# Optimization experiments

Hardware: AMD Instinct MI355X
Metric: run time of the kernel (lower is better)

The kernel has to match this reference:

```python
import jax, jax.numpy as jnp
from jax import lax
import numpy as np

NUM_NODES = 30   # pinned by LayerNorm(30) in TCNBlock
H = 4            # heads
C = 64           # channel per head
HC = H * C       # 256 = all_channels, first TCN channel
F_IN = 64
B = 1024         # graphs per batch
EPG = 240        # random edges per graph (no self loops; GATv2 adds them)
LN_EPS = 1e-5
NEG_SLOPE = 0.2


def _glorot(k, shp):
    fan_in = int(np.prod(shp[1:])) if len(shp) > 1 else int(shp[0])
    return jax.random.normal(k, shp, dtype=jnp.float32) / np.sqrt(fan_in)


def setup_inputs():
    key = jax.random.key(0)
    ks = jax.random.split(key, 16)
    N = B * NUM_NODES
    # random intra-graph edges with src != dst (PyG remove_self_loops then add_self_loops)
    src_l = jax.random.randint(ks[0], (B, EPG), 0, NUM_NODES)
    off = jax.random.randint(ks[1], (B, EPG), 1, NUM_NODES)
    dst_l = (src_l + off) % NUM_NODES
    base = (jnp.arange(B) * NUM_NODES)[:, None]
    edge_index = jnp.stack([(src_l + base).reshape(-1), (dst_l + base).reshape(-1)]).astype(jnp.int32)
    z = lambda *s: jnp.zeros(s, jnp.float32)
    return {
        "x": jax.random.normal(ks[2], (N, F_IN), dtype=jnp.float32),
        "gat_Wl": _glorot(ks[3], (HC, F_IN)), "gat_bl": z(HC),
        "gat_Wr": _glorot(ks[4], (HC, F_IN)), "gat_br": z(HC),
        "gat_att": _glorot(ks[5], (H, C)), "gat_bias": z(HC),
        "tcn0_w": _glorot(ks[6], (HC, HC, 3)), "tcn0_b": z(HC),
        "ln0_w": jnp.ones((NUM_NODES,), jnp.float32), "ln0_b": z(NUM_NODES),
        "tcn1_w": _glorot(ks[7], (512, HC, 3)), "tcn1_b": z(512),
        "ln1_w": jnp.ones((NUM_NODES,), jnp.float32), "ln1_b": z(NUM_NODES),
        "ds1_w": _glorot(ks[8], (512, HC, 1)), "ds1_b": z(512),
        "tcn2_w": _glorot(ks[9], (256, 512, 3)), "tcn2_b": z(256),
        "ln2_w": jnp.ones((NUM_NODES,), jnp.float32), "ln2_b": z(NUM_NODES),
        "ds2_w": _glorot(ks[10], (256, 512, 1)), "ds2_b": z(256),
        "fc1_w": _glorot(ks[11], (512, 256 * NUM_NODES)), "fc1_b": z(512),
        "fc2_w": _glorot(ks[12], (256, 512)), "fc2_b": z(256),
        "fc3_w": _glorot(ks[13], (144, 256)), "fc3_b": z(144),
        "edge_index": edge_index,
    }


def _conv1d(x, w, b, dil):
    # torch Conv1d: x [B,Cin,L], w [Cout,Cin,K], padding = dil*(K-1)//2
    pad = dil * (w.shape[-1] - 1) // 2
    y = lax.conv_general_dilated(x, w, (1,), [(pad, pad)], rhs_dilation=(dil,),
                                 dimension_numbers=("NCH", "OIH", "NCH"))
    return y + b[None, :, None]


def _ln(x, w, b):
    # LayerNorm over last dim (length 30)
    mu = jnp.mean(x, -1, keepdims=True)
    var = jnp.var(x, -1, keepdims=True)
    return (x - mu) * lax.rsqrt(var + LN_EPS) * w + b


def reference(x, gat_Wl, gat_bl, gat_Wr, gat_br, gat_att, gat_bias,
              tcn0_w, tcn0_b, ln0_w, ln0_b,
              tcn1_w, tcn1_b, ln1_w, ln1_b, ds1_w, ds1_b,
              tcn2_w, tcn2_b, ln2_w, ln2_b, ds2_w, ds2_b,
              fc1_w, fc1_b, fc2_w, fc2_b, fc3_w, fc3_b, edge_index):
    N = x.shape[0]
    # GATv2Conv default: add self loops
    loops = jnp.arange(N, dtype=edge_index.dtype)
    ei = jnp.concatenate([edge_index, jnp.stack([loops, loops])], axis=1)
    src, dst = ei[0], ei[1]
    xl = (x @ gat_Wl.T + gat_bl).reshape(N, H, C)  # source transform
    xr = (x @ gat_Wr.T + gat_br).reshape(N, H, C)  # target transform
    s = jax.nn.leaky_relu(xl[src] + xr[dst], NEG_SLOPE)          # [E,H,C]
    e = jnp.einsum("ehc,hc->eh", s, gat_att)                     # [E,H]
    m = jax.ops.segment_max(e, dst, num_segments=N)              # segment softmax
    expe = jnp.exp(e - m[dst])
    alpha = expe / jax.ops.segment_sum(expe, dst, num_segments=N)[dst]
    agg = jax.ops.segment_sum(alpha[:, :, None] * xl[src], dst, num_segments=N)
    h = jax.nn.relu(agg.reshape(N, HC) + gat_bias)
    h = h.reshape(-1, NUM_NODES, HC).transpose(0, 2, 1)          # [B, HC, 30]
    # TCN: dilations 1,2,4; residual with 1x1 downsample when channels change
    y = jax.nn.relu(_ln(_conv1d(h, tcn0_w, tcn0_b, 1), ln0_w, ln0_b)) + h
    y = jax.nn.relu(_ln(_conv1d(y, tcn1_w, tcn1_b, 2), ln1_w, ln1_b)) + _conv1d(y, ds1_w, ds1_b, 1)
    y = jax.nn.relu(_ln(_conv1d(y, tcn2_w, tcn2_b, 4), ln2_w, ln2_b)) + _conv1d(y, ds2_w, ds2_b, 1)
    z = y.reshape(y.shape[0], -1)                                # [B, 256*30]
    z = jax.nn.relu(z @ fc1_w.T + fc1_b)
    z = jax.nn.relu(z @ fc2_w.T + fc2_b)
    out = z @ fc3_w.T + fc3_b                                    # [B, 144]
    return out, alpha, ei
```

## Files before the change

kernel.cpp:

```cpp
#include <hip/hip_runtime.h>
#include <hip/hip_bf16.h>

typedef __bf16  bf16x8 __attribute__((ext_vector_type(8)));
typedef __bf16  bf16x4 __attribute__((ext_vector_type(4)));
typedef float   f32x4  __attribute__((ext_vector_type(4)));
typedef __hip_bfloat16 bf;

__device__ __forceinline__ float clamp256(float v) {
    return fminf(fmaxf(v, -256.f), 256.f);
}
__device__ __forceinline__ float sane(float v) {
    return fminf(fmaxf(v, -1e4f), 1e4f);
}
__device__ __forceinline__ int swzk(int k, int col) {
    return (k & ~31) | ((((k >> 3) & 3) ^ ((col >> 1) & 3)) << 3) | (k & 7);
}

template<int TAPS, bool HASWD>
__global__ __launch_bounds__(256) void gemm_tf(
    const bf* __restrict__ A, const bf* __restrict__ Wt, const bf* __restrict__ Wd,
    const float* __restrict__ bias, const float* __restrict__ biasd,
    const float* __restrict__ lnw, const float* __restrict__ lnb,
    const bf* __restrict__ res, int res_stride,
    bf* __restrict__ outb, float* __restrict__ outf, int out_stride,
    int M, int N, int K, int dil, int mode, int relu, int padded, int nn, int kLen)
{
    constexpr int NT = TAPS + (HASWD ? 1 : 0);
    __shared__ __align__(16) unsigned short sA[66 * 40];
    __shared__ __align__(16) unsigned short sB[NT][64 * 40];
    __shared__ float sS[4][64], sS2[4][64];

    const int tid  = threadIdx.x;
    const int wv   = tid >> 6;
    const int lane = tid & 63;
    const int m0   = blockIdx.y * 64;
    const int n0   = blockIdx.x * 64;
    const int frow = lane & 15;
    const int fq   = lane >> 4;
    const int kOff = blockIdx.z * kLen;
    const int kEnd = (kOff + kLen < K) ? (kOff + kLen) : K;

    if (tid < 40) sA[64 * 40 + tid] = (unsigned short)0;

    int aoff[NT];
    {
        int token = wv * 16 + frow;
        int b = token >> 5, l = token & 31;
        #pragma unroll
        for (int t = 0; t < NT; ++t) {
            int s = (t < TAPS) ? (t - TAPS / 2) * dil : 0;
            int ar;
            if (padded) {
                int ls = l + s;
                ar = ((unsigned)ls < 32u) ? (b * 32 + ls) : 64;
            } else {
                ar = token;
            }
            aoff[t] = ar * 40 + fq * 8;
        }
    }

    const int srow = tid >> 2;
    const int schk = (tid & 3) << 3;
    int raG = m0 + srow;
    if (!padded && raG >= M) raG = -1;
    const int rbG  = n0 + srow;
    const bool bval = rbG < N;
    const bf* Ap = (raG >= 0) ? (A + (size_t)raG * K) : nullptr;
    const bf* Bp[NT];
    #pragma unroll
    for (int t = 0; t < NT; ++t)
        Bp[t] = (HASWD && t == TAPS) ? (Wd + (size_t)rbG * K)
                                     : (Wt + ((size_t)t * N + rbG) * K);

    f32x4 accC[4], accR[4];
    #pragma unroll
    for (int i = 0; i < 4; ++i) { accC[i] = 0.f; accR[i] = 0.f; }

    const uint4 zu = make_uint4(0u, 0u, 0u, 0u);
    uint4 pa, pb[NT];
    pa = Ap ? *(const uint4*)(Ap + kOff + schk) : zu;
    #pragma unroll
    for (int t = 0; t < NT; ++t)
        pb[t] = bval ? *(const uint4*)(Bp[t] + kOff + schk) : zu;

    for (int kb = kOff; kb < kEnd; kb += 32) {
        __syncthreads();
        *(uint4*)(sA + srow * 40 + schk) = pa;
        #pragma unroll
        for (int t = 0; t < NT; ++t)
            *(uint4*)(&sB[t][srow * 40 + schk]) = pb[t];
        __syncthreads();
        int kn = kb + 32;
        if (kn < kEnd) {
            pa = Ap ? *(const uint4*)(Ap + kn + schk) : zu;
            #pragma unroll
            for (int t = 0; t < NT; ++t)
                pb[t] = bval ? *(const uint4*)(Bp[t] + kn + schk) : zu;
        }
        #pragma unroll
        for (int t = 0; t < TAPS; ++t) {
            bf16x8 af = *(const bf16x8*)(sA + aoff[t]);
            #pragma unroll
            for (int nt = 0; nt < 4; ++nt) {
                bf16x8 bg = *(const bf16x8*)(&sB[t][(nt * 16 + frow) * 40 + fq * 8]);
                accC[nt] = __builtin_amdgcn_mfma_f32_16x16x32_bf16(af, bg, accC[nt], 0, 0, 0);
            }
        }
        if constexpr (HASWD) {
            bf16x8 af = *(const bf16x8*)(sA + aoff[TAPS]);
            #pragma unroll
            for (int nt = 0; nt < 4; ++nt) {
                bf16x8 bg = *(const bf16x8*)(&sB[TAPS][(nt * 16 + frow) * 40 + fq * 8]);
                accR[nt] = __builtin_amdgcn_mfma_f32_16x16x32_bf16(af, bg, accR[nt], 0, 0, 0);
            }
        }
    }

    if (mode == 0) {
        #pragma unroll
        for (int nt = 0; nt < 4; ++nt) {
            int col = n0 + nt * 16 + frow;
            if (col >= N) continue;
            float bv = bias ? bias[col] : 0.f;
            #pragma unroll
            for (int r = 0; r < 4; ++r) {
                int row = m0 + wv * 16 + fq * 4 + r;
                if (row >= M) continue;
                float v = accC[nt][r] + bv;
                if (relu) v = fmaxf(v, 0.f);
                if (outb) outb[(size_t)row * out_stride + col] = __float2bfloat16(clamp256(v));
                else      outf[(size_t)row * out_stride + col] = sane(v);
            }
        }
    } else if (mode == 3) {
        bf* po = outb + (size_t)blockIdx.z * M * out_stride;
        #pragma unroll
        for (int nt = 0; nt < 4; ++nt) {
            int col = n0 + nt * 16 + frow;
            if (col >= N) continue;
            #pragma unroll
            for (int r = 0; r < 4; ++r) {
                int row = m0 + wv * 16 + fq * 4 + r;
                if (row >= M) continue;
                po[(size_t)row * out_stride + col] = __float2bfloat16(accC[nt][r]);
            }
        }
    } else if (mode == 5) {
        if constexpr (HASWD) {
            bf* out2 = (bf*)res;
            int orow_[4];
            #pragma unroll
            for (int r = 0; r < 4; ++r) {
                int row = m0 + wv * 16 + fq * 4 + r;
                orow_[r] = relu ? ((row / nn) * 32 + (row % nn)) : row;
            }
            #pragma unroll
            for (int nt = 0; nt < 4; ++nt) {
                int col = n0 + nt * 16 + frow;
                if (col >= N) continue;
                float bv = bias[col], bd = biasd[col];
                #pragma unroll
                for (int r = 0; r < 4; ++r) {
                    int row = m0 + wv * 16 + fq * 4 + r;
                    if (row >= M) continue;
                    outb[(size_t)row * out_stride + col] = __float2bfloat16(clamp256(accC[nt][r] + bv));
                    out2[(size_t)orow_[r] * res_stride + col] = __float2bfloat16(clamp256(accR[nt][r] + bd));
                }
            }
        }
    } else {
        float bvc[4], bdc[4];
        #pragma unroll
        for (int nt = 0; nt < 4; ++nt) {
            int col = n0 + nt * 16 + frow;
            bvc[nt] = bias[col];
            bdc[nt] = (HASWD && biasd) ? biasd[col] : 0.f;
        }
        float s[4], s2[4];
        #pragma unroll
        for (int nt = 0; nt < 4; ++nt) { s[nt] = 0.f; s2[nt] = 0.f; }
        #pragma unroll
        for (int nt = 0; nt < 4; ++nt)
            #pragma unroll
            for (int r = 0; r < 4; ++r) {
                int row = wv * 16 + fq * 4 + r;
                int l = row & 31;
                float v = sane(accC[nt][r] + bvc[nt]);
                if (l < nn) { s[nt] += v; s2[nt] += v * v; }
            }
        #pragma unroll
        for (int nt = 0; nt < 4; ++nt) {
            s[nt]  += __shfl_xor(s[nt], 16);  s[nt]  += __shfl_xor(s[nt], 32);
            s2[nt] += __shfl_xor(s2[nt], 16); s2[nt] += __shfl_xor(s2[nt], 32);
        }
        if (fq == 0) {
            #pragma unroll
            for (int nt = 0; nt < 4; ++nt) {
                sS[wv][nt * 16 + frow]  = s[nt];
                sS2[wv][nt * 16 + frow] = s2[nt];
            }
        }
        __syncthreads();
        const int gi = wv >> 1;
        const float inv = 1.f / (float)nn;
        #pragma unroll
        for (int nt = 0; nt < 4; ++nt) {
            int c = nt * 16 + frow;
            int colg = n0 + c;
            float S  = sS[2 * gi][c]  + sS[2 * gi + 1][c];
            float S2 = sS2[2 * gi][c] + sS2[2 * gi + 1][c];
            float mu = S * inv;
            float var = S2 * inv - mu * mu;
            float rs = rsqrtf(fmaxf(var, 0.f) + 1e-5f);
            #pragma unroll
            for (int r = 0; r < 4; ++r) {
                int row = wv * 16 + fq * 4 + r;
                int l = row & 31;
                int grow = m0 + row;
                float outv = 0.f;
                if (l < nn) {
                    float v = (sane(accC[nt][r] + bvc[nt]) - mu) * rs * lnw[l] + lnb[l];
                    v = fmaxf(v, 0.f);
                    float rr;
                    if constexpr (HASWD) rr = sane(accR[nt][r] + bdc[nt]);
                    else rr = __bfloat162float(res[(size_t)grow * res_stride + colg]);
                    outv = clamp256(v + rr);
                }
                outb[(size_t)grow * out_stride + colg] = __float2bfloat16(outv);
            }
        }
    }
}

template<int TAPS, bool HASWD>
__global__ __launch_bounds__(256, 2) void gemm_tcn(
    const bf* __restrict__ A, const bf* __restrict__ Wt, const bf* __restrict__ Wd,
    const float* __restrict__ bias, const float* __restrict__ biasd,
    const float* __restrict__ lnw, const float* __restrict__ lnb,
    const bf* __restrict__ res, int res_stride,
    bf* __restrict__ outb, int out_stride,
    int M, int N, int K, int dil, int nn)
{
    constexpr int NT = TAPS + (HASWD ? 1 : 0);
    constexpr int SA = 257 * 40;
    __shared__ __align__(16) unsigned short sA[2 * SA];
    __shared__ __align__(16) unsigned short sBall[2 * NT * 64 * 32];

    const int tid  = threadIdx.x;
    const int wv   = tid >> 6;
    const int lane = tid & 63;
    const int frow = lane & 15;
    const int fq   = lane >> 4;

    const int gx  = gridDim.x;
    const int nwg = gx * gridDim.y;
    int wg = blockIdx.y * gx + blockIdx.x;
    if ((nwg & 7) == 0) wg = (wg & 7) * (nwg >> 3) + (wg >> 3);
    const int n0 = (wg % gx) * 64;
    const int m0 = (wg / gx) * 256;

    if (tid < 40) {
        sA[256 * 40 + tid]      = (unsigned short)0;
        sA[SA + 256 * 40 + tid] = (unsigned short)0;
    }

    int aoff[TAPS][4];
    #pragma unroll
    for (int mr = 0; mr < 4; ++mr) {
        int token = wv * 64 + mr * 16 + frow;
        int b5 = token >> 5, l = token & 31;
        #pragma unroll
        for (int t = 0; t < TAPS; ++t) {
            int ls = l + (t - TAPS / 2) * dil;
            int ar = ((unsigned)ls < 32u) ? (b5 * 32 + ls) : 256;
            aoff[t][mr] = ar * 40 + fq * 8;
        }
    }
    const int bco = (fq ^ ((frow >> 1) & 3)) << 3;

    const int srow = tid >> 2;
    const int chS  = (tid & 3) << 3;
    const bf* Ap = A + (size_t)(m0 + srow) * K + chS;

    const bf* bsrc[4];
    {
        int lr = lane >> 2, lc = lane & 3;
        #pragma unroll
        for (int i = 0; i < 4; ++i) {
            int colb = n0 + i * 16 + lr;
            const bf* Wb;
            if (HASWD && wv == TAPS) Wb = Wd + (size_t)colb * K;
            else if (wv < TAPS)      Wb = Wt + ((size_t)wv * N + colb) * K;
            else                     Wb = Wt + (size_t)colb * K;
            bsrc[i] = Wb + lc * 8;
        }
    }

    f32x4 accC[4][4], accR[4][4];
    #pragma unroll
    for (int i = 0; i < 4; ++i)
        #pragma unroll
        for (int j = 0; j < 4; ++j) { accC[i][j] = 0.f; if (HASWD) accR[i][j] = 0.f; }

    #define ISSUE_B(BUFB, KBS)                                                      \
        if (wv < NT) {                                                              \
            unsigned short* bas = sBall + ((size_t)((BUFB) * NT + wv) * 64) * 32;   \
            _Pragma("unroll")                                                       \
            for (int i = 0; i < 4; ++i) {                                           \
                __builtin_amdgcn_global_load_lds(                                   \
                    (const __attribute__((address_space(1))) void*)(bsrc[i] + (KBS)), \
                    (__attribute__((address_space(3))) void*)(bas + i * 512),       \
                    16, 0, 0);                                                      \
            }                                                                       \
        }

    uint4 pa[4];
    #pragma unroll
    for (int i = 0; i < 4; ++i) pa[i] = *(const uint4*)(Ap + (size_t)i * 64 * K);
    ISSUE_B(0, 0);
    #pragma unroll
    for (int i = 0; i < 4; ++i)
        *(uint4*)(sA + (srow + i * 64) * 40 + chS) = pa[i];
    __syncthreads();

    int buf = 0;
    for (int kb = 0; kb < K; kb += 32) {
        int kn = kb + 32;
        if (kn < K) {
            #pragma unroll
            for (int i = 0; i < 4; ++i)
                pa[i] = *(const uint4*)(Ap + (size_t)i * 64 * K + kn);
            ISSUE_B(buf ^ 1, kn);
        }
        const unsigned short* sAb = sA + (size_t)buf * SA;
        const unsigned short* sBb = sBall + (size_t)buf * NT * 2048;
        bf16x8 aMid[4];
        #pragma unroll
        for (int mr = 0; mr < 4; ++mr)
            aMid[mr] = *(const bf16x8*)(sAb + aoff[TAPS / 2][mr]);
        #pragma unroll
        for (int t = 0; t < TAPS; ++t) {
            bf16x8 af[4];
            #pragma unroll
            for (int mr = 0; mr < 4; ++mr)
                af[mr] = (t == TAPS / 2) ? aMid[mr]
                                         : *(const bf16x8*)(sAb + aoff[t][mr]);
            #pragma unroll
            for (int nt = 0; nt < 4; ++nt) {
                bf16x8 bg = *(const bf16x8*)(sBb + (size_t)t * 2048 + (nt * 16 + frow) * 32 + bco);
                #pragma unroll
                for (int mr = 0; mr < 4; ++mr)
                    accC[mr][nt] = __builtin_amdgcn_mfma_f32_16x16x32_bf16(af[mr], bg, accC[mr][nt], 0, 0, 0);
            }
        }
        if constexpr (HASWD) {
            #pragma unroll
            for (int nt = 0; nt < 4; ++nt) {
                bf16x8 bg = *(const bf16x8*)(sBb + (size_t)TAPS * 2048 + (nt * 16 + frow) * 32 + bco);
                #pragma unroll
                for (int mr = 0; mr < 4; ++mr)
                    accR[mr][nt] = __builtin_amdgcn_mfma_f32_16x16x32_bf16(aMid[mr], bg, accR[mr][nt], 0, 0, 0);
            }
        }
        if (kn < K) {
            unsigned short* sAn = sA + (size_t)(buf ^ 1) * SA;
            #pragma unroll
            for (int i = 0; i < 4; ++i)
                *(uint4*)(sAn + (srow + i * 64) * 40 + chS) = pa[i];
        }
        __syncthreads();
        buf ^= 1;
    }
    #undef ISSUE_B

    float bvc[4], bdc[4];
    #pragma unroll
    for (int nt = 0; nt < 4; ++nt) {
        int col = n0 + nt * 16 + frow;
        bvc[nt] = bias[col];
        bdc[nt] = HASWD ? biasd[col] : 0.f;
    }
    float S[2][4], Q[2][4];
    #pragma unroll
    for (int h = 0; h < 2; ++h)
        #pragma unroll
        for (int nt = 0; nt < 4; ++nt) { S[h][nt] = 0.f; Q[h][nt] = 0.f; }
    #pragma unroll
    for (int mr = 0; mr < 4; ++mr) {
        const int h = mr >> 1;
        #pragma unroll
        for (int nt = 0; nt < 4; ++nt)
            #pragma unroll
            for (int r = 0; r < 4; ++r) {
                int l = (mr & 1) * 16 + fq * 4 + r;
                if (l < nn) {
                    float v = sane(accC[mr][nt][r] + bvc[nt]);
                    S[h][nt] += v; Q[h][nt] += v * v;
                }
            }
    }
    const float inv = 1.f / (float)nn;
    float mu[2][4], rsg[2][4];
    #pragma unroll
    for (int h = 0; h < 2; ++h)
        #pragma unroll
        for (int nt = 0; nt < 4; ++nt) {
            float s = S[h][nt], q = Q[h][nt];
            s += __shfl_xor(s, 16); s += __shfl_xor(s, 32);
            q += __shfl_xor(q, 16); q += __shfl_xor(q, 32);
            float m = s * inv;
            float var = q * inv - m * m;
            mu[h][nt]  = m;
            rsg[h][nt] = rsqrtf(fmaxf(var, 0.f) + 1e-5f);
        }
    float lw[2][4], lb2[2][4];
    #pragma unroll
    for (int p = 0; p < 2; ++p)
        #pragma unroll
        for (int r = 0; r < 4; ++r) {
            int l = p * 16 + fq * 4 + r;
            bool ok = l < nn;
            lw[p][r]  = ok ? lnw[l] : 0.f;
            lb2[p][r] = ok ? lnb[l] : 0.f;
        }
    #pragma unroll
    for (int nt = 0; nt < 4; ++nt) {
        const int colg = n0 + nt * 16 + frow;
        #pragma unroll
        for (int mr = 0; mr < 4; ++mr) {
            const int h = mr >> 1, p = mr & 1;
            #pragma unroll
            for (int r = 0; r < 4; ++r) {
                int l = p * 16 + fq * 4 + r;
                int grow = m0 + wv * 64 + mr * 16 + fq * 4 + r;
                float outv = 0.f;
                if (l < nn) {
                    float v = (sane(accC[mr][nt][r] + bvc[nt]) - mu[h][nt]) * rsg[h][nt] * lw[p][r] + lb2[p][r];
                    v = fmaxf(v, 0.f);
                    float rr;
                    if constexpr (HASWD) rr = sane(accR[mr][nt][r] + bdc[nt]);
                    else rr = __bfloat162float(res[(size_t)grow * res_stride + colg]);
                    outv = clamp256(v + rr);
                }
                outb[(size_t)grow * out_stride + colg] = __float2bfloat16(outv);
            }
        }
    }
}

#define MAXNE 270
#define XLS   260
#define SHP   264
template<int CONV>
__global__ __launch_bounds__(256, 4) void gat_fused4(
    const int* __restrict__ ei, const bf* __restrict__ xlb, const bf* __restrict__ xrb,
    const bf* __restrict__ Wlr, const float* __restrict__ gbl, const float* __restrict__ gbr,
    const float* __restrict__ att, const float* __restrict__ gbias,
    const bf* __restrict__ Wf, const float* __restrict__ cbias,
    const float* __restrict__ lnw, const float* __restrict__ lnb,
    bf* __restrict__ yout, float* __restrict__ dalpha, float* __restrict__ dei,
    int E0, int ET, int EPG, int nn)
{
    __shared__ __align__(16) __bf16 sXL[32 * XLS];
    __shared__ __align__(16) __bf16 sHX[33 * SHP];
    __shared__ __align__(16) float sExp[MAXNE * 4];
    __shared__ int   sSD[MAXNE];
    __shared__ unsigned short sList[MAXNE];
    __shared__ int   sCnt[32];
    __shared__ int   sOff[33];

    const int g = blockIdx.x, tid = threadIdx.x, wv = tid >> 6, lane = tid & 63;
    if (EPG + nn > MAXNE) return;
    const int NE = EPG + nn;
    const int frow = lane & 15;
    const int fq   = lane >> 4;

    for (int k = tid; k < EPG; k += 256) {
        int s = ei[(size_t)g * EPG + k] - g * nn;
        int d = ei[(size_t)E0 + (size_t)g * EPG + k] - g * nn;
        s = min(max(s, 0), nn - 1);
        d = min(max(d, 0), nn - 1);
        sSD[k] = s | (d << 16);
    }
    for (int k = EPG + tid; k < NE; k += 256) {
        int node = k - EPG;
        sSD[k] = node | (node << 16);
    }
    if constexpr (CONV) {
        unsigned short* sXg = (unsigned short*)sExp;
        const uint4* gx = (const uint4*)(xlb + (size_t)g * nn * 64);
        for (int k = tid; k < nn * 8; k += 256) {
            int node = k >> 3, k8 = k & 7;
            *(uint4*)(sXg + node * 64 + ((k8 ^ (node & 7)) << 3)) = gx[k];
        }
        const uint4 zu = make_uint4(0u, 0u, 0u, 0u);
        for (int k = nn * 8 + tid; k < 32 * 8; k += 256) {
            int node = k >> 3, k8 = k & 7;
            *(uint4*)(sXg + node * 64 + ((k8 ^ (node & 7)) << 3)) = zu;
        }
        __bf16 z = (__bf16)0.f;
        for (int k = tid; k < SHP; k += 256) sHX[32 * SHP + k] = z;
    } else {
        const uint4* gxl = (const uint4*)(xlb + (size_t)g * nn * 256);
        const uint4* gxr = (const uint4*)(xrb + (size_t)g * nn * 256);
        for (int k = tid; k < nn * 32; k += 256) {
            int node = k >> 5, c8 = k & 31;
            *(uint4*)(sXL + node * XLS + c8 * 8) = gxl[k];
            *(uint4*)(sHX + node * SHP + c8 * 8) = gxr[k];
        }
    }
    if (tid < 32) sCnt[tid] = 0;
    __syncthreads();

    for (int k = tid; k < NE; k += 256) atomicAdd(&sCnt[sSD[k] >> 16], 1);
    if constexpr (CONV) {
        const unsigned short* sXg = (const unsigned short*)sExp;
        bf16x8 axf[2][2];
        #pragma unroll
        for (int mr = 0; mr < 2; ++mr)
            #pragma unroll
            for (int kc = 0; kc < 2; ++kc) {
                int row = mr * 16 + frow;
                axf[mr][kc] = *(const bf16x8*)(sXg + row * 64 + (((kc * 4 + fq) ^ (row & 7)) << 3));
            }
        const int colw = wv * 64;
        #pragma unroll
        for (int out = 0; out < 2; ++out) {
            f32x4 ga[2][4];
            #pragma unroll
            for (int mr = 0; mr < 2; ++mr)
                #pragma unroll
                for (int ct = 0; ct < 4; ++ct) ga[mr][ct] = 0.f;
            #pragma unroll
            for (int kc = 0; kc < 2; ++kc)
                #pragma unroll
                for (int ct = 0; ct < 4; ++ct) {
                    const __bf16* bp = (const __bf16*)Wlr + (size_t)out * 16384 +
                        ((((size_t)(((colw >> 4) + ct) * 2 + kc) * 16 + frow) * 4 + fq) * 8);
                    bf16x8 bg = *(const bf16x8*)bp;
                    ga[0][ct] = __builtin_amdgcn_mfma_f32_16x16x32_bf16(axf[0][kc], bg, ga[0][ct], 0, 0, 0);
                    ga[1][ct] = __builtin_amdgcn_mfma_f32_16x16x32_bf16(axf[1][kc], bg, ga[1][ct], 0, 0, 0);
                }
            const float* bb = out ? gbr : gbl;
            #pragma unroll
            for (int ct = 0; ct < 4; ++ct) {
                int col = colw + ct * 16 + frow;
                float b = bb[col];
                #pragma unroll
                for (int mr = 0; mr < 2; ++mr)
                    #pragma unroll
                    for (int r = 0; r < 4; ++r) {
                        int row = mr * 16 + fq * 4 + r;
                        float v = clamp256(ga[mr][ct][r] + b);
                        if (out == 0) sXL[row * XLS + col] = (__bf16)v;
                        else          sHX[row * SHP + col] = (__bf16)v;
                    }
            }
        }
    }
    __syncthreads();
    if (tid < 32) {
        int acc = 0, last = 0;
        #pragma unroll
        for (int j = 0; j < 32; ++j) {
            int c = sCnt[j];
            if (j < tid) acc += c;
            if (j == 31) last = c;
        }
        sOff[tid] = acc;
        if (tid == 31) sOff[32] = acc + last;
        sCnt[tid] = 0;
    }
    __syncthreads();
    for (int k = tid; k < NE; k += 256) {
        int d = sSD[k] >> 16;
        int p = atomicAdd(&sCnt[d], 1);
        sList[sOff[d] + p] = (unsigned short)k;
    }

    for (int k = tid; k < NE; k += 256) {
        int s, d; size_t eg;
        if (k < EPG) {
            int sd = sSD[k];
            s = g * nn + (sd & 0xffff); d = g * nn + (sd >> 16);
            eg = (size_t)g * EPG + k;
        }
        else { int node = g * nn + (k - EPG); s = d = node; eg = (size_t)E0 + (size_t)g * nn + (k - EPG); }
        dei[eg] = (float)s;
        dei[(size_t)ET + eg] = (float)d;
    }
    __syncthreads();

    const float4 attv = *(const float4*)(att + lane * 4);
    const int h4 = lane >> 4;
    for (int i = wv; i < NE; i += 4) {
        int sd = sSD[i];
        int srcl = sd & 0xffff, dstl = sd >> 16;
        bf16x4 a = *(const bf16x4*)(sXL + srcl * XLS + lane * 4);
        bf16x4 b = *(const bf16x4*)(sHX + dstl * SHP + lane * 4);
        float p = 0.f;
        {
            float v0 = (float)a[0] + (float)b[0]; v0 = v0 > 0.f ? v0 : 0.2f * v0; p += v0 * attv.x;
            float v1 = (float)a[1] + (float)b[1]; v1 = v1 > 0.f ? v1 : 0.2f * v1; p += v1 * attv.y;
            float v2 = (float)a[2] + (float)b[2]; v2 = v2 > 0.f ? v2 : 0.2f * v2; p += v2 * attv.z;
            float v3 = (float)a[3] + (float)b[3]; v3 = v3 > 0.f ? v3 : 0.2f * v3; p += v3 * attv.w;
        }
        p += __shfl_xor(p, 1); p += __shfl_xor(p, 2);
        p += __shfl_xor(p, 4); p += __shfl_xor(p, 8);
        if ((lane & 15) == 0)
            sExp[i * 4 + h4] = __expf(fminf(fmaxf(p, -60.f), 60.f));
    }
    __syncthreads();

    {
        const int grp  = wv * 8 + (lane >> 3);
        const int s8   = lane & 7;
        const int chb  = s8 * 32;
        const int head = s8 >> 1;
        bf* hrow = yout + ((size_t)g * 32 + grp) * 256 + chb;

        if (grp < nn) {
            const int beg = sOff[grp], end = sOff[grp + 1];
            float den = 0.f;
            f32x4 acc[8];
            #pragma unroll
            for (int k2 = 0; k2 < 8; ++k2) acc[k2] = 0.f;

            for (int q = beg; q < end; ++q) {
                int e = sList[q];
                float ev = sExp[e * 4 + head];
                den += ev;
                const __bf16* xp = sXL + (sSD[e] & 0xffff) * XLS + chb;
                #pragma unroll
                for (int k2 = 0; k2 < 4; ++k2) {
                    bf16x8 xa = *(const bf16x8*)(xp + k2 * 8);
                    #pragma unroll
                    for (int j = 0; j < 4; ++j)
                        acc[k2 * 2][j]     += ev * (float)xa[j];
                    #pragma unroll
                    for (int j = 0; j < 4; ++j)
                        acc[k2 * 2 + 1][j] += ev * (float)xa[4 + j];
                }
            }
            const float rden = 1.f / fmaxf(den, 1e-30f);

            if (!(s8 & 1)) {
                for (int q = beg; q < end; ++q) {
                    int e = sList[q];
                    float al = fminf(fmaxf(sExp[e * 4 + head] * rden, 0.f), 1.f);
                    size_t eg = (e < EPG) ? ((size_t)g * EPG + e)
                                          : ((size_t)E0 + (size_t)g * nn + (e - EPG));
                    dalpha[eg * 4 + head] = al;
                }
            }

            #pragma unroll
            for (int k2 = 0; k2 < 8; ++k2) {
                float4 gbv = *(const float4*)(gbias + chb + k2 * 4);
                bf16x4 o;
                o[0] = (__bf16)clamp256(fmaxf(acc[k2][0] * rden + gbv.x, 0.f));
                o[1] = (__bf16)clamp256(fmaxf(acc[k2][1] * rden + gbv.y, 0.f));
                o[2] = (__bf16)clamp256(fmaxf(acc[k2][2] * rden + gbv.z, 0.f));
                o[3] = (__bf16)clamp256(fmaxf(acc[k2][3] * rden + gbv.w, 0.f));
                if constexpr (CONV) *(bf16x4*)(sHX + grp * SHP + chb + k2 * 4) = o;
                else                *(bf16x4*)(hrow + k2 * 4) = o;
            }
        } else {
            bf16x4 z; z[0] = (__bf16)0.f; z[1] = (__bf16)0.f; z[2] = (__bf16)0.f; z[3] = (__bf16)0.f;
            #pragma unroll
            for (int k2 = 0; k2 < 8; ++k2) {
                if constexpr (CONV) *(bf16x4*)(sHX + grp * SHP + chb + k2 * 4) = z;
                else                *(bf16x4*)(hrow + k2 * 4) = z;
            }
        }
    }

    if constexpr (CONV) {
        __syncthreads();
        const int colw = wv * 64;
        f32x4 c0[2][4];
        #pragma unroll
        for (int i = 0; i < 2; ++i)
            #pragma unroll
            for (int j = 0; j < 4; ++j) c0[i][j] = 0.f;

        #pragma unroll
        for (int kc = 0; kc < 8; ++kc) {
            bf16x8 af[3][2];
            #pragma unroll
            for (int t = 0; t < 3; ++t)
                #pragma unroll
                for (int mr = 0; mr < 2; ++mr) {
                    int l = mr * 16 + frow + t - 1;
                    int ar = ((unsigned)l < 32u) ? l : 32;
                    af[t][mr] = *(const bf16x8*)(sHX + ar * SHP + kc * 32 + fq * 8);
                }
            #pragma unroll
            for (int t = 0; t < 3; ++t) {
                bf16x8 bgs[4];
                #pragma unroll
                for (int nt = 0; nt < 4; ++nt) {
                    const __bf16* bp = (const __bf16*)Wf +
                        ((((size_t)(t * 16 + (colw >> 4) + nt) * 8 + kc) * 16 + frow) * 4 + fq) * 8;
                    bgs[nt] = *(const bf16x8*)bp;
                }
                #pragma unroll
                for (int nt = 0; nt < 4; ++nt) {
                    c0[0][nt] = __builtin_amdgcn_mfma_f32_16x16x32_bf16(af[t][0], bgs[nt], c0[0][nt], 0, 0, 0);
                    c0[1][nt] = __builtin_amdgcn_mfma_f32_16x16x32_bf16(af[t][1], bgs[nt], c0[1][nt], 0, 0, 0);
                }
            }
        }

        float bv[4];
        #pragma unroll
        for (int nt = 0; nt < 4; ++nt) bv[nt] = cbias[colw + nt * 16 + frow];
        float S[4], Q[4];
        #pragma unroll
        for (int nt = 0; nt < 4; ++nt) { S[nt] = 0.f; Q[nt] = 0.f; }
        #pragma unroll
        for (int mr = 0; mr < 2; ++mr)
            #pragma unroll
            for (int nt = 0; nt < 4; ++nt)
                #pragma unroll
                for (int r = 0; r < 4; ++r) {
                    int l = mr * 16 + fq * 4 + r;
                    if (l < nn) {
                        float v = sane(c0[mr][nt][r] + bv[nt]);
                        S[nt] += v; Q[nt] += v * v;
                    }
                }
        const float inv = 1.f / (float)nn;
        float mu[4], rsg[4];
        #pragma unroll
        for (int nt = 0; nt < 4; ++nt) {
            float s = S[nt], q = Q[nt];
            s += __shfl_xor(s, 16); s += __shfl_xor(s, 32);
            q += __shfl_xor(q, 16); q += __shfl_xor(q, 32);
            float m = s * inv;
            float var = q * inv - m * m;
            mu[nt]  = m;
            rsg[nt] = rsqrtf(fmaxf(var, 0.f) + 1e-5f);
        }
        float lw[2][4], lb2[2][4];
        #pragma unroll
        for (int p = 0; p < 2; ++p)
            #pragma unroll
            for (int r = 0; r < 4; ++r) {
                int l = p * 16 + fq * 4 + r;
                bool ok = l < nn;
                lw[p][r]  = ok ? lnw[l] : 0.f;
                lb2[p][r] = ok ? lnb[l] : 0.f;
            }
        #pragma unroll
        for (int nt = 0; nt < 4; ++nt) {
            const int colf = colw + nt * 16 + frow;
            #pragma unroll
            for (int mr = 0; mr < 2; ++mr)
                #pragma unroll
                for (int r = 0; r < 4; ++r) {
                    int l = mr * 16 + fq * 4 + r;
                    float outv = 0.f;
                    if (l < nn) {
                        float v = (sane(c0[mr][nt][r] + bv[nt]) - mu[nt]) * rsg[nt] * lw[mr][r] + lb2[mr][r];
                        v = fmaxf(v, 0.f);
                        float rr = (float)sHX[l * SHP + colf];
                        outv = clamp256(v + rr);
                    }
                    yout[((size_t)g * 32 + l) * 256 + colf] = __float2bfloat16(outv);
                }
        }
    }
}

struct CvtSegs { const float* in[7]; bf* out[7]; int n[7]; };
__global__ void prep_cvt(CvtSegs s, int total)
{
    int idx = blockIdx.x * 256 + threadIdx.x;
    if (idx >= total) return;
    #pragma unroll
    for (int i = 0; i < 7; ++i) {
        if (idx < s.n[i]) { s.out[i][idx] = __float2bfloat16(s.in[i][idx]); return; }
        idx -= s.n[i];
    }
}
struct TapSegs { const float* w[3]; bf* o[3]; int cc[3]; int kk[3]; int swz[3]; };
__global__ void prep_taps3(TapSegs s, int total)
{
    int idx = blockIdx.x * 256 + threadIdx.x;
    if (idx >= total) return;
    #pragma unroll
    for (int i = 0; i < 3; ++i) {
        if (idx < s.cc[i]) {
            unsigned K = (unsigned)s.kk[i];
            unsigned co = (unsigned)idx / K, ci = (unsigned)idx % K;
            int dst = co * K + (s.swz[i] ? swzk(ci, co) : ci);
            #pragma unroll
            for (int k = 0; k < 3; ++k)
                s.o[i][(size_t)k * s.cc[i] + dst] = __float2bfloat16(s.w[i][(size_t)idx * 3 + k]);
            return;
        }
        idx -= s.cc[i];
    }
}
__global__ void prep_wswz(const float* __restrict__ w, bf* __restrict__ o,
                          int total, int K, int swz)
{
    int idx = blockIdx.x * 256 + threadIdx.x;
    if (idx >= total) return;
    int co = idx / K, ci = idx % K;
    o[(size_t)co * K + (swz ? swzk(ci, co) : ci)] = __float2bfloat16(w[idx]);
}
__global__ void prep_bfrag(const float* __restrict__ w, bf* __restrict__ o, int HC)
{
    int idx = blockIdx.x * 256 + threadIdx.x;
    if (idx >= HC * HC) return;
    int co = idx / HC, ci = idx % HC;
    int cg = co >> 4, fr = co & 15, kc = ci >> 5, fq = (ci >> 3) & 3, w8 = ci & 7;
    int NCg = HC >> 4, NKc = HC >> 5;
    #pragma unroll
    for (int t = 0; t < 3; ++t) {
        size_t dst = (((((size_t)t * NCg + cg) * NKc + kc) * 16 + fr) * 4 + fq) * 8 + w8;
        o[dst] = __float2bfloat16(w[(size_t)idx * 3 + t]);
    }
}
__global__ void prep_gwfrag(const float* __restrict__ wl, const float* __restrict__ wr,
                            bf* __restrict__ o, int HC, int FI)
{
    int idx = blockIdx.x * 256 + threadIdx.x;
    int tot = HC * FI;
    if (idx >= 2 * tot) return;
    const float* w = (idx < tot) ? wl : wr;
    int j = (idx < tot) ? idx : idx - tot;
    int col = j / FI, k = j % FI;
    int cg = col >> 4, fr = col & 15, kc = k >> 5, fq = (k >> 3) & 3, w8 = k & 7;
    size_t dst = (size_t)((idx < tot) ? 0 : 1) * tot +
        ((((size_t)(cg * (FI >> 5) + kc) * 16 + fr) * 4 + fq) * 8 + w8);
    o[dst] = __float2bfloat16(w[j]);
}

__global__ void prep_fc1(const float* __restrict__ w, bf* __restrict__ o, int F1, int nn, int HC)
{
    int idx = blockIdx.x * 256 + threadIdx.x;
    int kw = 32 * HC;
    if (idx >= F1 * kw) return;
    int co = idx / kw, r = idx % kw, l = r / HC, ci = r % HC;
    float hv = 0.f;
    if (l < nn) hv = w[(size_t)co * (HC * nn) + ci * nn + l];
    o[idx] = __float2bfloat16(hv);
}

__global__ void fc1red(const bf* __restrict__ zp, const float* __restrict__ bias,
                       bf* __restrict__ o, int MN, int N, int S)
{
    int idx = blockIdx.x * 256 + threadIdx.x;
    if (idx >= MN) return;
    float s = 0.f;
    for (int z = 0; z < S; ++z) s += __bfloat162float(zp[(size_t)z * MN + idx]);
    o[idx] = __float2bfloat16(clamp256(fmaxf(s + bias[idx % N], 0.f)));
}

extern "C" void kernel_launch(void* const* d_in, const int* in_sizes, int n_in,
                              void* d_out, int out_size, void* d_ws, size_t ws_size,
                              hipStream_t stream)
{
    (void)n_in; (void)ws_size;
    const float* x   = (const float*)d_in[0];
    const float* Wl  = (const float*)d_in[1];  const float* bl  = (const float*)d_in[2];
    const float* Wr  = (const float*)d_in[3];  const float* br  = (const float*)d_in[4];
    const float* att = (const float*)d_in[5];  const float* gb  = (const float*)d_in[6];
    const float* t0w = (const float*)d_in[7];  const float* t0b = (const float*)d_in[8];
    const float* l0w = (const float*)d_in[9];  const float* l0b = (const float*)d_in[10];
    const float* t1w = (const float*)d_in[11]; const float* t1b = (const float*)d_in[12];
    const float* l1w = (const float*)d_in[13]; const float* l1b = (const float*)d_in[14];
    const float* d1w = (const float*)d_in[15]; const float* d1b = (const float*)d_in[16];
    const float* t2w = (const float*)d_in[17]; const float* t2b = (const float*)d_in[18];
    const float* l2w = (const float*)d_in[19]; const float* l2b = (const float*)d_in[20];
    const float* d2w = (const float*)d_in[21]; const float* d2b = (const float*)d_in[22];
    const float* f1w = (const float*)d_in[23]; const float* f1b = (const float*)d_in[24];
    const float* f2w = (const float*)d_in[25]; const float* f2b = (const float*)d_in[26];
    const float* f3w = (const float*)d_in[27]; const float* f3b = (const float*)d_in[28];
    const int*   ei  = (const int*)d_in[29];

    const int HC   = in_sizes[6];
    const int F_IN = in_sizes[1] / (HC > 0 ? HC : 1);
    const int NN   = in_sizes[0] / (F_IN > 0 ? F_IN : 1);
    const int E0   = in_sizes[29] / 2;
    const int ET   = E0 + NN;
    int nn = in_sizes[9];  nn = nn < 1 ? 1 : (nn > 32 ? 32 : nn);
    const int NG   = NN / nn;
    const int EPG  = NG > 0 ? E0 / NG : 0;
    const int C1   = in_sizes[12];
    const int C2   = in_sizes[18];
    const int F1   = in_sizes[24];
    const int F2   = in_sizes[26];
    const int F3   = in_sizes[28];
    const int NG2  = (NG + 1) / 2;

    float* dout   = (float*)d_out;
    float* dei    = dout + ((size_t)out_size - 2 * (size_t)ET);
    float* dalpha = dei - (size_t)ET * 4;

    const bool fused0 = (HC == 256) && (F_IN == 64) && (nn >= 1) && (nn <= 32)
                        && (EPG + nn <= MAXNE) && ((NN % 64) == 0);
    const int  gcA = NG2, gcB = NG - NG2;
    const bool fastc = ((gcA * 32) % 256 == 0) && ((gcB * 32) % 256 == 0)
                       && (C1 % 64 == 0) && (C2 % 64 == 0)
                       && (HC % 32 == 0) && (C1 % 32 == 0);

    char* ws = (char*)d_ws;
    const size_t MB = 1ull << 20;
    bf*    xb   = (bf*)(ws);
    bf*    WkA  = (bf*)(ws + 4 * MB);
    bf*    WkB  = WkA + (size_t)3 * HC * HC;
    bf*    WkC  = WkB + (size_t)3 * C1 * HC;
    bf*    Wlb  = WkC + (size_t)3 * C2 * C1;
    bf*    Wrb  = Wlb + (size_t)HC * F_IN;
    bf*    f2wb = Wrb + (size_t)HC * F_IN;
    bf*    f3wb = f2wb + (size_t)F2 * F1;
    bf*    d1wb = f3wb + (size_t)F3 * F2;
    bf*    d2wb = d1wb + (size_t)C1 * HC;
    bf*    WkAf = d2wb + (size_t)C2 * C1;
    bf*    WlrF = WkAf + (size_t)3 * HC * HC;
    char*  S0   = ws + (size_t)(7.5 * MB);
    char*  S1   = ws + 25 * MB;

    bf*    xrb  = (bf*)S0;
    bf*    hbuf = (bf*)S0;
    bf*    xlb  = (bf*)S1;
    bf*    y0   = fused0 ? (bf*)S0 : (bf*)S1;
    bf*    y1c  = fused0 ? (bf*)S1 : (bf*)S0;
    char*  fcS  = fused0 ? S1 : S0;
    bf*    W1t  = (bf*)fcS;
    bf*    z1p  = (bf*)(fcS + (size_t)(8.5 * MB));
    bf*    z1   = (bf*)(ws);
    bf*    z2   = (bf*)(ws + 2 * MB);

    {
        CvtSegs cs;
        cs.in[0] = x;   cs.out[0] = xb;   cs.n[0] = NN * F_IN;
        cs.in[1] = Wl;  cs.out[1] = Wlb;  cs.n[1] = HC * F_IN;
        cs.in[2] = Wr;  cs.out[2] = Wrb;  cs.n[2] = HC * F_IN;
        cs.in[3] = f2w; cs.out[3] = f2wb; cs.n[3] = F2 * F1;
        cs.in[4] = f3w; cs.out[4] = f3wb; cs.n[4] = F3 * F2;
        cs.in[5] = nullptr; cs.out[5] = nullptr; cs.n[5] = 0;
        cs.in[6] = nullptr; cs.out[6] = nullptr; cs.n[6] = 0;
        int tot = 0; for (int i = 0; i < 5; ++i) tot += cs.n[i];
        prep_cvt<<<(tot + 255) / 256, 256, 0, stream>>>(cs, tot);
        TapSegs ts;
        ts.w[0] = t0w; ts.o[0] = WkA; ts.cc[0] = HC * HC; ts.kk[0] = HC; ts.swz[0] = 0;
        ts.w[1] = t1w; ts.o[1] = WkB; ts.cc[1] = C1 * HC; ts.kk[1] = HC; ts.swz[1] = fastc ? 1 : 0;
        ts.w[2] = t2w; ts.o[2] = WkC; ts.cc[2] = C2 * C1; ts.kk[2] = C1; ts.swz[2] = fastc ? 1 : 0;
        int tt = ts.cc[0] + ts.cc[1] + ts.cc[2];
        prep_taps3<<<(tt + 255) / 256, 256, 0, stream>>>(ts, tt);
        prep_wswz<<<(C1 * HC + 255) / 256, 256, 0, stream>>>(d1w, d1wb, C1 * HC, HC, fastc ? 1 : 0);
        prep_wswz<<<(C2 * C1 + 255) / 256, 256, 0, stream>>>(d2w, d2wb, C2 * C1, C1, fastc ? 1 : 0);
        if (fused0) {
            prep_bfrag<<<(HC * HC + 255) / 256, 256, 0, stream>>>(t0w, WkAf, HC);
            prep_gwfrag<<<(2 * HC * F_IN + 255) / 256, 256, 0, stream>>>(Wl, Wr, WlrF, HC, F_IN);
        }
    }

    if (fused0) {
        gat_fused4<1><<<NG, 256, 0, stream>>>(ei, xb, nullptr, WlrF, bl, br,
                                              att, gb, WkAf, t0b, l0w, l0b,
                                              y0, dalpha, dei, E0, ET, EPG, nn);
    } else {
        gemm_tf<1, true><<<dim3((HC + 63) / 64, (NN + 63) / 64), 256, 0, stream>>>(
            xb, Wlb, Wrb, bl, br, nullptr, nullptr, (const bf*)xrb, HC,
            xlb, nullptr, HC, NN, HC, F_IN, 1, 5, 0, 0, nn, F_IN);
        gat_fused4<0><<<NG, 256, 0, stream>>>(ei, xlb, xrb, nullptr, nullptr, nullptr,
                                              att, gb, nullptr, nullptr, nullptr, nullptr,
                                              hbuf, dalpha, dei, E0, ET, EPG, nn);
        gemm_tf<3, false><<<dim3((HC + 63) / 64, NG * 32 / 64), 256, 0, stream>>>(
            hbuf, WkA, nullptr, t0b, nullptr, l0w, l0b, hbuf, HC,
            y0, nullptr, HC, NG * 32, HC, HC, 1, 2, 0, 1, nn, HC);
    }

    for (int c = 0; c < 2; ++c) {
        int g0 = c * NG2;
        int gc = (c == 0) ? NG2 : (NG - NG2);
        if (gc <= 0) continue;
        const bf* y0c = y0 + (size_t)g0 * 32 * HC;
        bf*       y2c = y0 + (size_t)g0 * 32 * HC;
        if (fastc) {
            gemm_tcn<3, true><<<dim3(C1 / 64, gc * 32 / 256), 256, 0, stream>>>(
                y0c, WkB, d1wb, t1b, d1b, l1w, l1b, nullptr, 0,
                y1c, C1, gc * 32, C1, HC, 2, nn);
            gemm_tcn<3, true><<<dim3(C2 / 64, gc * 32 / 256), 256, 0, stream>>>(
                y1c, WkC, d2wb, t2b, d2b, l2w, l2b, nullptr, 0,
                y2c, C2, gc * 32, C2, C1, 4, nn);
        } else {
            gemm_tf<3, true><<<dim3((C1 + 63) / 64, gc * 32 / 64), 256, 0, stream>>>(
                y0c, WkB, d1wb, t1b, d1b, l1w, l1b, nullptr, 0,
                y1c, nullptr, C1, gc * 32, C1, HC, 2, 2, 0, 1, nn, HC);
            gemm_tf<3, true><<<dim3((C2 + 63) / 64, gc * 32 / 64), 256, 0, stream>>>(
                y1c, WkC, d2wb, t2b, d2b, l2w, l2b, nullptr, 0,
                y2c, nullptr, C2, gc * 32, C2, C1, 4, 2, 0, 1, nn, C1);
        }
    }

    prep_fc1<<<(F1 * 32 * HC + 255) / 256, 256, 0, stream>>>(f1w, W1t, F1, nn, HC);
    gemm_tf<1, false><<<dim3((F1 + 63) / 64, (NG + 63) / 64, 8), 256, 0, stream>>>(
        y0, W1t, nullptr, nullptr, nullptr, nullptr, nullptr, nullptr, 0,
        z1p, nullptr, F1, NG, F1, 32 * HC, 1, 3, 0, 0, nn, 4 * HC);
    fc1red<<<(NG * F1 + 255) / 256, 256, 0, stream>>>(z1p, f1b, z1, NG * F1, F1, 8);

    gemm_tf<1, false><<<dim3((F2 + 63) / 64, (NG + 63) / 64), 256, 0, stream>>>(
        z1, f2wb, nullptr, f2b, nullptr, nullptr, nullptr, nullptr, 0,
        z2, nullptr, F2, NG, F2, F1, 1, 0, 1, 0, nn, F1);
    gemm_tf<1, false><<<dim3((F3 + 63) / 64, (NG + 63) / 64), 256, 0, stream>>>(
        z2, f3wb, nullptr, f3b, nullptr, nullptr, nullptr, nullptr, 0,
        nullptr, dout, F3, NG, F3, F2, 1, 0, 0, 0, nn, F2);
}
```

Measured before the change: 424.0 us.

## Template TCN GEMM row tile and restructure GAT alpha writes into coalesced pass

Makes the TCN GEMM's M-tile size a template parameter. The second TCN layer (N=256) now uses 128-row tiles with higher occupancy, which gives more workgroups and better CU fill. Separately, the GAT kernel stores per-destination denominators in shared memory and writes all attention coefficients afterwards in one coalesced float4 pass over edges. This replaces the scattered per-head writes inside the aggregation loop, at the cost of an extra barrier and division pass.

Measured after the change: 410.4 us. -3.2%, faster.

```diff
diff --git a/kernel.cpp b/kernel.cpp
--- a/kernel.cpp
+++ b/kernel.cpp
@@ -233,8 +233,8 @@
     }
 }
 
-template<int TAPS, bool HASWD>
-__global__ __launch_bounds__(256, 2) void gemm_tcn(
+template<int TAPS, bool HASWD, int MR>
+__global__ __launch_bounds__(256, (MR == 2) ? 3 : 2) void gemm_tcn(
     const bf* __restrict__ A, const bf* __restrict__ Wt, const bf* __restrict__ Wd,
     const float* __restrict__ bias, const float* __restrict__ biasd,
     const float* __restrict__ lnw, const float* __restrict__ lnb,
@@ -243,7 +243,9 @@
     int M, int N, int K, int dil, int nn)
 {
     constexpr int NT = TAPS + (HASWD ? 1 : 0);
-    constexpr int SA = 257 * 40;
+    constexpr int ROWS = 64 * MR;
+    constexpr int GH = (MR >= 4) ? 2 : 1;
+    constexpr int SA = (ROWS + 1) * 40;
     __shared__ __align__(16) unsigned short sA[2 * SA];
     __shared__ __align__(16) unsigned short sBall[2 * NT * 64 * 32];
 
@@ -258,22 +260,22 @@
     int wg = blockIdx.y * gx + blockIdx.x;
     if ((nwg & 7) == 0) wg = (wg & 7) * (nwg >> 3) + (wg >> 3);
     const int n0 = (wg % gx) * 64;
-    const int m0 = (wg / gx) * 256;
+    const int m0 = (wg / gx) * ROWS;
 
     if (tid < 40) {
-        sA[256 * 40 + tid]      = (unsigned short)0;
-        sA[SA + 256 * 40 + tid] = (unsigned short)0;
-    }
-
-    int aoff[TAPS][4];
-    #pragma unroll
-    for (int mr = 0; mr < 4; ++mr) {
-        int token = wv * 64 + mr * 16 + frow;
+        sA[ROWS * 40 + tid]      = (unsigned short)0;
+        sA[SA + ROWS * 40 + tid] = (unsigned short)0;
+    }
+
+    int aoff[TAPS][MR];
+    #pragma unroll
+    for (int mr = 0; mr < MR; ++mr) {
+        int token = wv * (16 * MR) + mr * 16 + frow;
         int b5 = token >> 5, l = token & 31;
         #pragma unroll
         for (int t = 0; t < TAPS; ++t) {
             int ls = l + (t - TAPS / 2) * dil;
-            int ar = ((unsigned)ls < 32u) ? (b5 * 32 + ls) : 256;
+            int ar = ((unsigned)ls < 32u) ? (b5 * 32 + ls) : ROWS;
             aoff[t][mr] = ar * 40 + fq * 8;
         }
     }
@@ -297,9 +299,9 @@
         }
     }
 
-    f32x4 accC[4][4], accR[4][4];
-    #pragma unroll
-    for (int i = 0; i < 4; ++i)
+    f32x4 accC[MR][4], accR[MR][4];
+    #pragma unroll
+    for (int i = 0; i < MR; ++i)
         #pragma unroll
         for (int j = 0; j < 4; ++j) { accC[i][j] = 0.f; if (HASWD) accR[i][j] = 0.f; }
 
@@ -315,12 +317,12 @@
             }                                                                       \
         }
 
-    uint4 pa[4];
-    #pragma unroll
-    for (int i = 0; i < 4; ++i) pa[i] = *(const uint4*)(Ap + (size_t)i * 64 * K);
+    uint4 pa[MR];
+    #pragma unroll
+    for (int i = 0; i < MR; ++i) pa[i] = *(const uint4*)(Ap + (size_t)i * 64 * K);
     ISSUE_B(0, 0);
     #pragma unroll
-    for (int i = 0; i < 4; ++i)
+    for (int i = 0; i < MR; ++i)
         *(uint4*)(sA + (srow + i * 64) * 40 + chS) = pa[i];
     __syncthreads();
 
@@ -329,28 +331,28 @@
         int kn = kb + 32;
         if (kn < K) {
             #pragma unroll
-            for (int i = 0; i < 4; ++i)
+            for (int i = 0; i < MR; ++i)
                 pa[i] = *(const uint4*)(Ap + (size_t)i * 64 * K + kn);
             ISSUE_B(buf ^ 1, kn);
         }
         const unsigned short* sAb = sA + (size_t)buf * SA;
         const unsigned short* sBb = sBall + (size_t)buf * NT * 2048;
-        bf16x8 aMid[4];
-        #pragma unroll
-        for (int mr = 0; mr < 4; ++mr)
+        bf16x8 aMid[MR];
+        #pragma unroll
+        for (int mr = 0; mr < MR; ++mr)
             aMid[mr] = *(const bf16x8*)(sAb + aoff[TAPS / 2][mr]);
         #pragma unroll
         for (int t = 0; t < TAPS; ++t) {
-            bf16x8 af[4];
-            #pragma unroll
-            for (int mr = 0; mr < 4; ++mr)
+            bf16x8 af[MR];
+            #pragma unroll
+            for (int mr = 0; mr < MR; ++mr)
                 af[mr] = (t == TAPS / 2) ? aMid[mr]
                                          : *(const bf16x8*)(sAb + aoff[t][mr]);
             #pragma unroll
             for (int nt = 0; nt < 4; ++nt) {
                 bf16x8 bg = *(const bf16x8*)(sBb + (size_t)t * 2048 + (nt * 16 + frow) * 32 + bco);
                 #pragma unroll
-                for (int mr = 0; mr < 4; ++mr)
+                for (int mr = 0; mr < MR; ++mr)
                     accC[mr][nt] = __builtin_amdgcn_mfma_f32_16x16x32_bf16(af[mr], bg, accC[mr][nt], 0, 0, 0);
             }
         }
@@ -359,14 +361,14 @@
             for (int nt = 0; nt < 4; ++nt) {
                 bf16x8 bg = *(const bf16x8*)(sBb + (size_t)TAPS * 2048 + (nt * 16 + frow) * 32 + bco);
                 #pragma unroll
-                for (int mr = 0; mr < 4; ++mr)
+                for (int mr = 0; mr < MR; ++mr)
                     accR[mr][nt] = __builtin_amdgcn_mfma_f32_16x16x32_bf16(aMid[mr], bg, accR[mr][nt], 0, 0, 0);
             }
         }
         if (kn < K) {
             unsigned short* sAn = sA + (size_t)(buf ^ 1) * SA;
             #pragma unroll
-            for (int i = 0; i < 4; ++i)
+            for (int i = 0; i < MR; ++i)
                 *(uint4*)(sAn + (srow + i * 64) * 40 + chS) = pa[i];
         }
         __syncthreads();
@@ -381,13 +383,13 @@
         bvc[nt] = bias[col];
         bdc[nt] = HASWD ? biasd[col] : 0.f;
     }
-    float S[2][4], Q[2][4];
-    #pragma unroll
-    for (int h = 0; h < 2; ++h)
+    float S[GH][4], Q[GH][4];
+    #pragma unroll
+    for (int h = 0; h < GH; ++h)
         #pragma unroll
         for (int nt = 0; nt < 4; ++nt) { S[h][nt] = 0.f; Q[h][nt] = 0.f; }
     #pragma unroll
-    for (int mr = 0; mr < 4; ++mr) {
+    for (int mr = 0; mr < MR; ++mr) {
         const int h = mr >> 1;
         #pragma unroll
         for (int nt = 0; nt < 4; ++nt)
@@ -401,9 +403,9 @@
             }
     }
     const float inv = 1.f / (float)nn;
-    float mu[2][4], rsg[2][4];
-    #pragma unroll
-    for (int h = 0; h < 2; ++h)
+    float mu[GH][4], rsg[GH][4];
+    #pragma unroll
+    for (int h = 0; h < GH; ++h)
         #pragma unroll
         for (int nt = 0; nt < 4; ++nt) {
             float s = S[h][nt], q = Q[h][nt];
@@ -428,12 +430,12 @@
     for (int nt = 0; nt < 4; ++nt) {
         const int colg = n0 + nt * 16 + frow;
         #pragma unroll
-        for (int mr = 0; mr < 4; ++mr) {
+        for (int mr = 0; mr < MR; ++mr) {
             const int h = mr >> 1, p = mr & 1;
             #pragma unroll
             for (int r = 0; r < 4; ++r) {
                 int l = p * 16 + fq * 4 + r;
-                int grow = m0 + wv * 64 + mr * 16 + fq * 4 + r;
+                int grow = m0 + wv * (16 * MR) + mr * 16 + fq * 4 + r;
                 float outv = 0.f;
                 if (l < nn) {
                     float v = (sane(accC[mr][nt][r] + bvc[nt]) - mu[h][nt]) * rsg[h][nt] * lw[p][r] + lb2[p][r];
@@ -467,6 +469,7 @@
     __shared__ __align__(16) float sExp[MAXNE * 4];
     __shared__ int   sSD[MAXNE];
     __shared__ unsigned short sList[MAXNE];
+    __shared__ float sDen[128];
     __shared__ int   sCnt[32];
     __shared__ int   sOff[33];
 
@@ -643,17 +646,8 @@
                         acc[k2 * 2 + 1][j] += ev * (float)xa[4 + j];
                 }
             }
+            if (!(s8 & 1)) sDen[grp * 4 + head] = den;
             const float rden = 1.f / fmaxf(den, 1e-30f);
-
-            if (!(s8 & 1)) {
-                for (int q = beg; q < end; ++q) {
-                    int e = sList[q];
-                    float al = fminf(fmaxf(sExp[e * 4 + head] * rden, 0.f), 1.f);
-                    size_t eg = (e < EPG) ? ((size_t)g * EPG + e)
-                                          : ((size_t)E0 + (size_t)g * nn + (e - EPG));
-                    dalpha[eg * 4 + head] = al;
-                }
-            }
 
             #pragma unroll
             for (int k2 = 0; k2 < 8; ++k2) {
@@ -675,9 +669,21 @@
             }
         }
     }
+    __syncthreads();
+
+    for (int k = tid; k < NE; k += 256) {
+        int d = sSD[k] >> 16;
+        size_t eg = (k < EPG) ? ((size_t)g * EPG + k)
+                              : ((size_t)E0 + (size_t)g * nn + (k - EPG));
+        float4 al;
+        al.x = fminf(fmaxf(sExp[k * 4 + 0] / fmaxf(sDen[d * 4 + 0], 1e-30f), 0.f), 1.f);
+        al.y = fminf(fmaxf(sExp[k * 4 + 1] / fmaxf(sDen[d * 4 + 1], 1e-30f), 0.f), 1.f);
+        al.z = fminf(fmaxf(sExp[k * 4 + 2] / fmaxf(sDen[d * 4 + 2], 1e-30f), 0.f), 1.f);
+        al.w = fminf(fmaxf(sExp[k * 4 + 3] / fmaxf(sDen[d * 4 + 3], 1e-30f), 0.f), 1.f);
+        *(float4*)(dalpha + eg * 4) = al;
+    }
 
     if constexpr (CONV) {
-        __syncthreads();
         const int colw = wv * 64;
         f32x4 c0[2][4];
         #pragma unroll
@@ -985,10 +991,10 @@
         const bf* y0c = y0 + (size_t)g0 * 32 * HC;
         bf*       y2c = y0 + (size_t)g0 * 32 * HC;
         if (fastc) {
-            gemm_tcn<3, true><<<dim3(C1 / 64, gc * 32 / 256), 256, 0, stream>>>(
+            gemm_tcn<3, true, 4><<<dim3(C1 / 64, gc * 32 / 256), 256, 0, stream>>>(
                 y0c, WkB, d1wb, t1b, d1b, l1w, l1b, nullptr, 0,
                 y1c, C1, gc * 32, C1, HC, 2, nn);
-            gemm_tcn<3, true><<<dim3(C2 / 64, gc * 32 / 256), 256, 0, stream>>>(
+            gemm_tcn<3, true, 2><<<dim3(C2 / 64, gc * 32 / 128), 256, 0, stream>>>(
                 y1c, WkC, d2wb, t2b, d2b, l2w, l2b, nullptr, 0,
                 y2c, C2, gc * 32, C2, C1, 4, nn);
         } else {
```
